# Kernel tuning notes

Hardware: AMD Instinct MI355X
Metric: run time of the kernel (lower is better)

## Reference

```python
import jax, jax.numpy as jnp
import numpy as np

K = 3          # conv kernel size
STRIDE = 1     # conv stride (SAME padding)
ITERS = 3      # DR routing iterations
EPS = 1e-9     # squash epsilon


def squash(s, axis):
    # v = ||s||^2 / (1 + ||s||^2) * s / ||s||   (DR squash)
    sq = jnp.sum(s * s, axis=axis, keepdims=True)
    return (sq / (1.0 + sq)) * s * jax.lax.rsqrt(sq + EPS)


def setup_inputs() -> dict:
    key = jax.random.key(0)
    k1, k2, k3 = jax.random.split(key, 3)
    b, h, w, iCaps, iPose = 8, 12, 12, 32, 16
    oCaps, oPose = 32, 16
    x = jax.random.normal(k1, (b, h, w, iCaps, iPose), dtype=jnp.float32)
    # Wa: [kk*iCaps, oCaps, iPose, oPose] (leading 1 of the TF weight is dropped)
    fan = K * K * iCaps * iPose
    W = jax.random.normal(k2, (K * K * iCaps, oCaps, iPose, oPose), dtype=jnp.float32) * np.float32(np.sqrt(2.0 / fan))
    # biases: [oCaps, oPose] (TF shape [1,1,oCaps,oPose,1], broadcastable)
    biases = jax.random.normal(k3, (oCaps, oPose), dtype=jnp.float32) * 0.05
    return {"x": x, "W": W, "biases": biases}


def _kernel_tile(x2d):
    # im2col for SAME padding, stride 1.  x2d: (b, h, w, C) -> (b, h, w, k*k, C)
    b, h, w, C = x2d.shape
    pad = K // 2
    xp = jnp.pad(x2d, ((0, 0), (pad, pad), (pad, pad), (0, 0)))
    patches = jnp.stack(
        [xp[:, i:i + h, j:j + w, :] for i in range(K) for j in range(K)], axis=3
    )
    return patches  # (b, h, w, k*k, C)


def reference(x, W, biases):
    b, h, w, iCaps, iPose = x.shape
    iC = K * K * iCaps
    oC, oP = biases.shape

    # 1. kernel_tile: gather k*k neighborhoods
    patches = _kernel_tile(x.reshape(b, h, w, iCaps * iPose))      # (b,h,w,kk,iCaps*iPose)
    u = patches.reshape(b * h * w, iC, iPose)                       # (bx, iC, iPose)

    # 2. transform_view (vector capsules): votes[n,i,c,:] = u[n,i,:] @ W[i,c,:,:]
    votes = jnp.einsum('nip,icpq->nicq', u, W)                      # (bx, iC, oC, oP)

    # 3. DR routing
    bx = votes.shape[0]
    logits = jnp.zeros((bx, iC, oC), dtype=votes.dtype)
    v = None
    for ii in range(ITERS):
        c = jax.nn.softmax(logits, axis=2)                          # coupling coeffs over oCaps
        s = jnp.einsum('nic,nicq->ncq', c, votes) + biases          # (bx, oC, oP)
        v = squash(s, axis=2)
        if ii < ITERS - 1:
            logits = logits + jnp.einsum('nicq,ncq->nic', votes, v)  # agreement

    return v.reshape(b, h, w, oC, oP)
```

## Files before the change

### kernel.cpp

```cpp
#include <hip/hip_runtime.h>
#include <stdint.h>

typedef unsigned short ushort_t;

#define KK3 3
#define IC 32
#define IP 16
#define OC 32
#define OP 16
#define NI 288
#define HH 12
#define WWW 12
#define NTOT 1152
#define CQ 512
#define EPSQ 1e-9f
#define RWAVES 4
#define RSTEPS 36
#define NIP 144
#define NIG 18
#define IPG 8
#define SROW 132
#define SPAR (16 * SROW)
#define SWAVE (2 * SPAR)

typedef __attribute__((ext_vector_type(8))) short bf16x8;
typedef __attribute__((ext_vector_type(4))) float f32x4;

__device__ __forceinline__ float bf_lo(unsigned u) { return __uint_as_float(u << 16); }
__device__ __forceinline__ float bf_hi(unsigned u) { return __uint_as_float(u & 0xffff0000u); }
__device__ __forceinline__ ushort_t f2bf(float f) {
    unsigned u = __float_as_uint(f);
    return (ushort_t)((u + 0x7fffu + ((u >> 16) & 1u)) >> 16);
}

__global__ __launch_bounds__(64) void pack_kernel(
    const float* __restrict__ W, ushort_t* __restrict__ Wp)
{
    const int blk = blockIdx.x;
    const int ip = blk >> 5;
    const int c = blk & 31;
    const int l = threadIdx.x;
    const int i = ip * 2 + ((l >> 5) & 1);
    const int p0 = ((l >> 4) & 1) * 8;
    const int q = l & 15;
    const float* src = W + (((size_t)(i * 32 + c) * 16 + p0) * 16 + q);
    union { ushort_t s[8]; uint4 u4; } o;
#pragma unroll
    for (int j = 0; j < 8; ++j) o.s[j] = f2bf(src[(size_t)j * 16]);
    *(uint4*)(Wp + ((size_t)blk * 64 + l) * 8) = o.u4;
}

__global__ __launch_bounds__(256) void votes_s0_kernel(
    const float* __restrict__ x, const ushort_t* __restrict__ Wp,
    ushort_t* __restrict__ votes, float* __restrict__ s0_part,
    int nStart, int nCount)
{
    __shared__ ushort_t slab[4 * SWAVE];

    const int t = threadIdx.x;
    const int w = t >> 6;
    const int l = t & 63;
    const int pxt = blockIdx.x;
    const int ig = blockIdx.y;

    const int n = nStart + pxt * 16 + (l & 15);
    const int b = n / (HH * WWW);
    const int rem = n % (HH * WWW);
    const int y = rem / WWW;
    const int xx = rem % WWW;
    const int ioff = (l >> 5) & 1;
    const int p0 = ((l >> 4) & 1) * 8;

    const int q = l & 15;
    const int r0 = (l >> 4) * 4;
    const int j16 = l & 15;
    const int g4 = l >> 4;

    ushort_t* const myslab = slab + w * SWAVE;

    const bf16x8 z8 = {0, 0, 0, 0, 0, 0, 0, 0};
    const f32x4 z4 = {0.f, 0.f, 0.f, 0.f};

    f32x4 accs0[8];
#pragma unroll
    for (int ctl = 0; ctl < 8; ++ctl) accs0[ctl] = z4;

    for (int m = 0; m < IPG; ++m) {
        const int ip = ig * IPG + m;
        union { ushort_t s[8]; bf16x8 v; } ua;
        {
            const int i = ip * 2 + ioff;
            const int ky = i / (KK3 * IC);
            const int kx = (i / IC) % KK3;
            const int ic = i & (IC - 1);
            const int sy = y + ky - 1;
            const int sx = xx + kx - 1;
            if (sy >= 0 && sy < HH && sx >= 0 && sx < WWW) {
                const float* s = x + ((((size_t)b * HH + sy) * WWW + sx) * IC + ic) * IP + p0;
                const float4 v0 = *(const float4*)s;
                const float4 v1 = *(const float4*)(s + 4);
                ua.s[0] = f2bf(v0.x); ua.s[1] = f2bf(v0.y); ua.s[2] = f2bf(v0.z); ua.s[3] = f2bf(v0.w);
                ua.s[4] = f2bf(v1.x); ua.s[5] = f2bf(v1.y); ua.s[6] = f2bf(v1.z); ua.s[7] = f2bf(v1.w);
            } else {
#pragma unroll
                for (int j = 0; j < 8; ++j) ua.s[j] = 0;
            }
        }

#pragma unroll
        for (int ctl = 0; ctl < 8; ++ctl) {
            const int ct = w * 8 + ctl;
            const bf16x8 frag = *(const bf16x8*)(Wp + (((size_t)ip * 32 + ct) * 64 + l) * 8);
            const bf16x8 be = (l < 32) ? frag : z8;
            const bf16x8 bo = (l < 32) ? z8 : frag;
            const f32x4 ve = __builtin_amdgcn_mfma_f32_16x16x32_bf16(ua.v, be, z4, 0, 0, 0);
            const f32x4 vo = __builtin_amdgcn_mfma_f32_16x16x32_bf16(ua.v, bo, z4, 0, 0, 0);
            accs0[ctl] = __builtin_amdgcn_mfma_f32_16x16x32_bf16(ua.v, frag, accs0[ctl], 0, 0, 0);
#pragma unroll
            for (int r = 0; r < 4; ++r) {
                myslab[(r0 + r) * SROW + ctl * 16 + q] = f2bf(ve[r]);
                myslab[SPAR + (r0 + r) * SROW + ctl * 16 + q] = f2bf(vo[r]);
            }
        }

#pragma unroll
        for (int s = 0; s < 2; ++s) {
#pragma unroll
            for (int h = 0; h < 4; ++h) {
                const int row = h * 4 + g4;
                const ushort_t* sp = myslab + s * SPAR + row * SROW + j16 * 8;
                const uint2 lo = *(const uint2*)sp;
                const uint2 hi = *(const uint2*)(sp + 4);
                ushort_t* dst = votes + ((size_t)(pxt * 16 + row) * NI + (2 * ip + s)) * CQ
                                + w * 128 + j16 * 8;
                uint4 o; o.x = lo.x; o.y = lo.y; o.z = hi.x; o.w = hi.y;
                *(uint4*)dst = o;
            }
        }
    }

    {
#pragma unroll
        for (int ctl = 0; ctl < 8; ++ctl) {
            const int cq = (w * 8 + ctl) * 16 + q;
#pragma unroll
            for (int r = 0; r < 4; ++r)
                s0_part[((size_t)ig * nCount + pxt * 16 + r0 + r) * CQ + cq] = accs0[ctl][r];
        }
    }
}

#define UNPACK16(A, B)                                                     \
    const float f0 = bf_lo(A.x), f1 = bf_hi(A.x), f2 = bf_lo(A.y),         \
                f3 = bf_hi(A.y), f4 = bf_lo(A.z), f5 = bf_hi(A.z),         \
                f6 = bf_lo(A.w), f7 = bf_hi(A.w), f8 = bf_lo(B.x),         \
                f9 = bf_hi(B.x), f10 = bf_lo(B.y), f11 = bf_hi(B.y),       \
                f12 = bf_lo(B.z), f13 = bf_hi(B.z), f14 = bf_lo(B.w),      \
                f15 = bf_hi(B.w);

__global__ __launch_bounds__(256) void route_kernel(
    const ushort_t* __restrict__ votes, const float* __restrict__ s0_part,
    const float* __restrict__ bias, float* __restrict__ out,
    int nStart, int nCount)
{
    __shared__ float sPart[RWAVES][CQ];
    __shared__ float s_sh[CQ];
    __shared__ float vcur_sh[CQ];
    __shared__ float fac_sh[OC];
    __shared__ float pad_lds[5632];

    const int bn = blockIdx.x;
    const int t = threadIdx.x;
    ((volatile float*)pad_lds)[t] = 0.f;

    const int wv = t >> 6;
    const int l = t & 63;
    const int isub = l >> 5;
    const int c = l & 31;
    const int iBase = 2 * wv + isub;

    const ushort_t* pbase = votes + (size_t)bn * NI * CQ + (size_t)iBase * CQ + c * OP;
    const size_t stepB = (size_t)8 * CQ;

#pragma unroll
    for (int rep = 0; rep < 2; ++rep) {
        const int k = t + rep * 256;
        float s = 0.f;
#pragma unroll
        for (int g = 0; g < NIG; ++g)
            s += s0_part[((size_t)g * nCount + bn) * CQ + k];
        s_sh[k] = fmaf(s, 1.0f / OC, bias[k]);
    }
    __syncthreads();
    if (t < OC) {
        float sq = 0.f;
#pragma unroll
        for (int q = 0; q < OP; ++q) { const float s = s_sh[t * OP + q]; sq = fmaf(s, s, sq); }
        fac_sh[t] = (sq / (1.0f + sq)) * rsqrtf(sq + EPSQ);
    }
    __syncthreads();
#pragma unroll
    for (int rep = 0; rep < 2; ++rep) {
        const int k = t + rep * 256;
        vcur_sh[k] = s_sh[k] * fac_sh[k >> 4];
    }
    __syncthreads();

    float sa[16];
    float vr[16];

#define RBODY(AA, BB)                                                       \
        {                                                                   \
            UNPACK16(AA, BB)                                                \
            float a = f0 * vr[0];                                           \
            a = fmaf(f1, vr[1], a);   a = fmaf(f2, vr[2], a);               \
            a = fmaf(f3, vr[3], a);   a = fmaf(f4, vr[4], a);               \
            a = fmaf(f5, vr[5], a);   a = fmaf(f6, vr[6], a);               \
            a = fmaf(f7, vr[7], a);   a = fmaf(f8, vr[8], a);               \
            a = fmaf(f9, vr[9], a);   a = fmaf(f10, vr[10], a);             \
            a = fmaf(f11, vr[11], a); a = fmaf(f12, vr[12], a);             \
            a = fmaf(f13, vr[13], a); a = fmaf(f14, vr[14], a);             \
            a = fmaf(f15, vr[15], a);                                       \
            const float e = __expf(a);                                      \
            float es = e;                                                   \
            es += __shfl_xor(es, 1);                                        \
            es += __shfl_xor(es, 2);                                        \
            es += __shfl_xor(es, 4);                                        \
            es += __shfl_xor(es, 8);                                        \
            es += __shfl_xor(es, 16);                                       \
            const float coup = __fdividef(e, es);                           \
            sa[0] = fmaf(coup, f0, sa[0]);   sa[1] = fmaf(coup, f1, sa[1]); \
            sa[2] = fmaf(coup, f2, sa[2]);   sa[3] = fmaf(coup, f3, sa[3]); \
            sa[4] = fmaf(coup, f4, sa[4]);   sa[5] = fmaf(coup, f5, sa[5]); \
            sa[6] = fmaf(coup, f6, sa[6]);   sa[7] = fmaf(coup, f7, sa[7]); \
            sa[8] = fmaf(coup, f8, sa[8]);   sa[9] = fmaf(coup, f9, sa[9]); \
            sa[10] = fmaf(coup, f10, sa[10]); sa[11] = fmaf(coup, f11, sa[11]); \
            sa[12] = fmaf(coup, f12, sa[12]); sa[13] = fmaf(coup, f13, sa[13]); \
            sa[14] = fmaf(coup, f14, sa[14]); sa[15] = fmaf(coup, f15, sa[15]); \
        }
#define RPREF(AA, BB, rn)                                                   \
        if ((rn) < RSTEPS) {                                                \
            const uint4* pn = (const uint4*)(pbase + (size_t)(rn) * stepB); \
            AA = pn[0]; BB = pn[1];                                         \
        }

#pragma unroll
    for (int it = 0; it < 2; ++it) {
#pragma unroll
        for (int k = 0; k < 4; ++k) {
            const float4 v4 = *(const float4*)&vcur_sh[c * 16 + 4 * k];
            vr[4*k] = v4.x; vr[4*k+1] = v4.y; vr[4*k+2] = v4.z; vr[4*k+3] = v4.w;
        }
#pragma unroll
        for (int q = 0; q < 16; ++q) sa[q] = 0.f;

        uint4 A0, B0, A1, B1, A2, B2, A3, B3, A4, B4, A5, B5;
        RPREF(A0, B0, 0)
        RPREF(A1, B1, 1)
        RPREF(A2, B2, 2)
        RPREF(A3, B3, 3)
        RPREF(A4, B4, 4)
        RPREF(A5, B5, 5)
        for (int r = 0; r < RSTEPS; r += 6) {
            RBODY(A0, B0) RPREF(A0, B0, r + 6)
            RBODY(A1, B1) RPREF(A1, B1, r + 7)
            RBODY(A2, B2) RPREF(A2, B2, r + 8)
            RBODY(A3, B3) RPREF(A3, B3, r + 9)
            RBODY(A4, B4) RPREF(A4, B4, r + 10)
            RBODY(A5, B5) RPREF(A5, B5, r + 11)
        }

#pragma unroll
        for (int q = 0; q < 16; ++q) sa[q] += __shfl_xor(sa[q], 32);
        if (isub == 0) {
#pragma unroll
            for (int k = 0; k < 4; ++k)
                *(float4*)&sPart[wv][c * 16 + 4 * k] = make_float4(sa[4*k], sa[4*k+1], sa[4*k+2], sa[4*k+3]);
        }
        __syncthreads();
#pragma unroll
        for (int rep = 0; rep < 2; ++rep) {
            const int k = t + rep * 256;
            float s = (sPart[0][k] + sPart[1][k]) + (sPart[2][k] + sPart[3][k]);
            s_sh[k] = s + bias[k];
        }
        __syncthreads();
        if (t < OC) {
            float sq = 0.f;
#pragma unroll
            for (int q = 0; q < OP; ++q) { const float s = s_sh[t * OP + q]; sq = fmaf(s, s, sq); }
            fac_sh[t] = (sq / (1.0f + sq)) * rsqrtf(sq + EPSQ);
        }
        __syncthreads();
        if (it == 0) {
#pragma unroll
            for (int rep = 0; rep < 2; ++rep) {
                const int k = t + rep * 256;
                vcur_sh[k] += s_sh[k] * fac_sh[k >> 4];
            }
            __syncthreads();
        } else {
#pragma unroll
            for (int rep = 0; rep < 2; ++rep) {
                const int k = t + rep * 256;
                out[(size_t)(nStart + bn) * CQ + k] = s_sh[k] * fac_sh[k >> 4];
            }
        }
    }
}

extern "C" void kernel_launch(void* const* d_in, const int* in_sizes, int n_in,
                              void* d_out, int out_size, void* d_ws, size_t ws_size,
                              hipStream_t stream)
{
    const float* x = (const float*)d_in[0];
    const float* Wg = (const float*)d_in[1];
    const float* bias = (const float*)d_in[2];
    float* out = (float*)d_out;

    const size_t perN = (size_t)NI * CQ * sizeof(ushort_t);
    const size_t packBytes = (size_t)NIP * 32 * 64 * 8 * 2;
    const size_t perNpart = (size_t)NIG * CQ * sizeof(float);

    int chunk = 768;
    if (ws_size < (size_t)chunk * (perN + perNpart) + packBytes) {
        size_t avail = (ws_size > packBytes) ? ws_size - packBytes : 0;
        chunk = (int)(avail / (perN + perNpart));
        chunk &= ~15;
        if (chunk < 16) chunk = 16;
    }
    const size_t packOff = (size_t)chunk * perN;
    const size_t partOff = packOff + packBytes;

    ushort_t* votes = (ushort_t*)d_ws;
    ushort_t* Wp = (ushort_t*)((char*)d_ws + packOff);
    float* s0_part = (float*)((char*)d_ws + partOff);

    hipLaunchKernelGGL(pack_kernel, dim3(NIP * 32), dim3(64), 0, stream, Wg, Wp);

    for (int start = 0; start < NTOT; start += chunk) {
        const int cnt = (NTOT - start < chunk) ? (NTOT - start) : chunk;
        hipLaunchKernelGGL(votes_s0_kernel, dim3(cnt / 16, NIG), dim3(256), 0, stream,
                           x, Wp, votes, s0_part, start, cnt);
        hipLaunchKernelGGL(route_kernel, dim3(cnt), dim3(256), 0, stream,
                           votes, s0_part, bias, out, start, cnt);
    }
}
```

Measured before the change: 246.4 us.

## Split routing into per-iteration sweep kernels over two input-capsule halves

The single route kernel, which ran both routing iterations per pixel in one block, is replaced by two sweep-kernel launches. Each launch uses a grid of pixels by two halves of the 288 input capsules, so twice as many blocks share the votes reads. Per-half partial sums go through global workspace buffers and a small final kernel applies bias and squash. This raises parallelism and occupancy at the cost of extra launches, extra global traffic for partials, and recomputing the initial s0 reduction in every block.

```diff
diff --git a/kernel.cpp b/kernel.cpp
--- a/kernel.cpp
+++ b/kernel.cpp
@@ -15,7 +15,7 @@
 #define CQ 512
 #define EPSQ 1e-9f
 #define RWAVES 4
-#define RSTEPS 36
+#define RSTEPS 18
 #define NIP 144
 #define NIG 18
 #define IPG 8
@@ -158,10 +158,10 @@
                 f12 = bf_lo(B.z), f13 = bf_hi(B.z), f14 = bf_lo(B.w),      \
                 f15 = bf_hi(B.w);
 
-__global__ __launch_bounds__(256) void route_kernel(
+__global__ __launch_bounds__(256) void sweep_kernel(
     const ushort_t* __restrict__ votes, const float* __restrict__ s0_part,
-    const float* __restrict__ bias, float* __restrict__ out,
-    int nStart, int nCount)
+    const float* __restrict__ sIn_part, float* __restrict__ sOut_part,
+    const float* __restrict__ bias, int it, int nCount)
 {
     __shared__ float sPart[RWAVES][CQ];
     __shared__ float s_sh[CQ];
@@ -170,6 +170,7 @@
     __shared__ float pad_lds[5632];
 
     const int bn = blockIdx.x;
+    const int h = blockIdx.y;
     const int t = threadIdx.x;
     ((volatile float*)pad_lds)[t] = 0.f;
 
@@ -179,7 +180,8 @@
     const int c = l & 31;
     const int iBase = 2 * wv + isub;
 
-    const ushort_t* pbase = votes + (size_t)bn * NI * CQ + (size_t)iBase * CQ + c * OP;
+    const ushort_t* pbase = votes + (size_t)bn * NI * CQ
+                            + (size_t)(h * 144 + iBase) * CQ + c * OP;
     const size_t stepB = (size_t)8 * CQ;
 
 #pragma unroll
@@ -205,9 +207,39 @@
         vcur_sh[k] = s_sh[k] * fac_sh[k >> 4];
     }
     __syncthreads();
+    if (it == 1) {
+#pragma unroll
+        for (int rep = 0; rep < 2; ++rep) {
+            const int k = t + rep * 256;
+            const float s = sIn_part[(size_t)bn * CQ + k]
+                          + sIn_part[((size_t)nCount + bn) * CQ + k] + bias[k];
+            s_sh[k] = s;
+        }
+        __syncthreads();
+        if (t < OC) {
+            float sq = 0.f;
+#pragma unroll
+            for (int q = 0; q < OP; ++q) { const float s = s_sh[t * OP + q]; sq = fmaf(s, s, sq); }
+            fac_sh[t] = (sq / (1.0f + sq)) * rsqrtf(sq + EPSQ);
+        }
+        __syncthreads();
+#pragma unroll
+        for (int rep = 0; rep < 2; ++rep) {
+            const int k = t + rep * 256;
+            vcur_sh[k] += s_sh[k] * fac_sh[k >> 4];
+        }
+        __syncthreads();
+    }
 
     float sa[16];
     float vr[16];
+#pragma unroll
+    for (int k = 0; k < 4; ++k) {
+        const float4 v4 = *(const float4*)&vcur_sh[c * 16 + 4 * k];
+        vr[4*k] = v4.x; vr[4*k+1] = v4.y; vr[4*k+2] = v4.z; vr[4*k+3] = v4.w;
+    }
+#pragma unroll
+    for (int q = 0; q < 16; ++q) sa[q] = 0.f;
 
 #define RBODY(AA, BB)                                                       \
         {                                                                   \
@@ -244,69 +276,68 @@
             AA = pn[0]; BB = pn[1];                                         \
         }
 
-#pragma unroll
-    for (int it = 0; it < 2; ++it) {
-#pragma unroll
-        for (int k = 0; k < 4; ++k) {
-            const float4 v4 = *(const float4*)&vcur_sh[c * 16 + 4 * k];
-            vr[4*k] = v4.x; vr[4*k+1] = v4.y; vr[4*k+2] = v4.z; vr[4*k+3] = v4.w;
-        }
-#pragma unroll
-        for (int q = 0; q < 16; ++q) sa[q] = 0.f;
-
-        uint4 A0, B0, A1, B1, A2, B2, A3, B3, A4, B4, A5, B5;
-        RPREF(A0, B0, 0)
-        RPREF(A1, B1, 1)
-        RPREF(A2, B2, 2)
-        RPREF(A3, B3, 3)
-        RPREF(A4, B4, 4)
-        RPREF(A5, B5, 5)
-        for (int r = 0; r < RSTEPS; r += 6) {
-            RBODY(A0, B0) RPREF(A0, B0, r + 6)
-            RBODY(A1, B1) RPREF(A1, B1, r + 7)
-            RBODY(A2, B2) RPREF(A2, B2, r + 8)
-            RBODY(A3, B3) RPREF(A3, B3, r + 9)
-            RBODY(A4, B4) RPREF(A4, B4, r + 10)
-            RBODY(A5, B5) RPREF(A5, B5, r + 11)
-        }
-
-#pragma unroll
-        for (int q = 0; q < 16; ++q) sa[q] += __shfl_xor(sa[q], 32);
-        if (isub == 0) {
-#pragma unroll
-            for (int k = 0; k < 4; ++k)
-                *(float4*)&sPart[wv][c * 16 + 4 * k] = make_float4(sa[4*k], sa[4*k+1], sa[4*k+2], sa[4*k+3]);
-        }
-        __syncthreads();
-#pragma unroll
-        for (int rep = 0; rep < 2; ++rep) {
-            const int k = t + rep * 256;
-            float s = (sPart[0][k] + sPart[1][k]) + (sPart[2][k] + sPart[3][k]);
-            s_sh[k] = s + bias[k];
-        }
-        __syncthreads();
-        if (t < OC) {
-            float sq = 0.f;
-#pragma unroll
-            for (int q = 0; q < OP; ++q) { const float s = s_sh[t * OP + q]; sq = fmaf(s, s, sq); }
-            fac_sh[t] = (sq / (1.0f + sq)) * rsqrtf(sq + EPSQ);
-        }
-        __syncthreads();
-        if (it == 0) {
-#pragma unroll
-            for (int rep = 0; rep < 2; ++rep) {
-                const int k = t + rep * 256;
-                vcur_sh[k] += s_sh[k] * fac_sh[k >> 4];
-            }
-            __syncthreads();
-        } else {
-#pragma unroll
-            for (int rep = 0; rep < 2; ++rep) {
-                const int k = t + rep * 256;
-                out[(size_t)(nStart + bn) * CQ + k] = s_sh[k] * fac_sh[k >> 4];
-            }
-        }
-    }
+    uint4 A0, B0, A1, B1, A2, B2, A3, B3, A4, B4, A5, B5;
+    RPREF(A0, B0, 0)
+    RPREF(A1, B1, 1)
+    RPREF(A2, B2, 2)
+    RPREF(A3, B3, 3)
+    RPREF(A4, B4, 4)
+    RPREF(A5, B5, 5)
+    for (int r = 0; r < RSTEPS; r += 6) {
+        RBODY(A0, B0) RPREF(A0, B0, r + 6)
+        RBODY(A1, B1) RPREF(A1, B1, r + 7)
+        RBODY(A2, B2) RPREF(A2, B2, r + 8)
+        RBODY(A3, B3) RPREF(A3, B3, r + 9)
+        RBODY(A4, B4) RPREF(A4, B4, r + 10)
+        RBODY(A5, B5) RPREF(A5, B5, r + 11)
+    }
+
+#pragma unroll
+    for (int q = 0; q < 16; ++q) sa[q] += __shfl_xor(sa[q], 32);
+    if (isub == 0) {
+#pragma unroll
+        for (int k = 0; k < 4; ++k)
+            *(float4*)&sPart[wv][c * 16 + 4 * k] = make_float4(sa[4*k], sa[4*k+1], sa[4*k+2], sa[4*k+3]);
+    }
+    __syncthreads();
+#pragma unroll
+    for (int rep = 0; rep < 2; ++rep) {
+        const int k = t + rep * 256;
+        sOut_part[((size_t)h * nCount + bn) * CQ + k] =
+            (sPart[0][k] + sPart[1][k]) + (sPart[2][k] + sPart[3][k]);
+    }
+}
+
+__global__ __launch_bounds__(64) void final_kernel(
+    const float* __restrict__ sIn_part, const float* __restrict__ bias,
+    float* __restrict__ out, int nStart, int nCount)
+{
+    const int bn = blockIdx.x;
+    const int l = threadIdx.x;
+    const int base = (l >> 1) * 16 + (l & 1) * 8;
+
+    float s[8];
+    {
+        const float4 a0 = *(const float4*)&sIn_part[(size_t)bn * CQ + base];
+        const float4 a1 = *(const float4*)&sIn_part[(size_t)bn * CQ + base + 4];
+        const float4 b0 = *(const float4*)&sIn_part[((size_t)nCount + bn) * CQ + base];
+        const float4 b1 = *(const float4*)&sIn_part[((size_t)nCount + bn) * CQ + base + 4];
+        const float4 c0 = *(const float4*)&bias[base];
+        const float4 c1 = *(const float4*)&bias[base + 4];
+        s[0] = a0.x + b0.x + c0.x; s[1] = a0.y + b0.y + c0.y;
+        s[2] = a0.z + b0.z + c0.z; s[3] = a0.w + b0.w + c0.w;
+        s[4] = a1.x + b1.x + c1.x; s[5] = a1.y + b1.y + c1.y;
+        s[6] = a1.z + b1.z + c1.z; s[7] = a1.w + b1.w + c1.w;
+    }
+    float sq = 0.f;
+#pragma unroll
+    for (int j = 0; j < 8; ++j) sq = fmaf(s[j], s[j], sq);
+    sq += __shfl_xor(sq, 1);
+    const float fac = (sq / (1.0f + sq)) * rsqrtf(sq + EPSQ);
+    float4 o0 = make_float4(s[0] * fac, s[1] * fac, s[2] * fac, s[3] * fac);
+    float4 o1 = make_float4(s[4] * fac, s[5] * fac, s[6] * fac, s[7] * fac);
+    *(float4*)&out[(size_t)(nStart + bn) * CQ + base] = o0;
+    *(float4*)&out[(size_t)(nStart + bn) * CQ + base + 4] = o1;
 }
 
 extern "C" void kernel_launch(void* const* d_in, const int* in_sizes, int n_in,
@@ -321,20 +352,25 @@
     const size_t perN = (size_t)NI * CQ * sizeof(ushort_t);
     const size_t packBytes = (size_t)NIP * 32 * 64 * 8 * 2;
     const size_t perNpart = (size_t)NIG * CQ * sizeof(float);
+    const size_t perNsw = (size_t)4 * CQ * sizeof(float);
 
     int chunk = 768;
-    if (ws_size < (size_t)chunk * (perN + perNpart) + packBytes) {
+    if (ws_size < (size_t)chunk * (perN + perNpart + perNsw) + packBytes) {
         size_t avail = (ws_size > packBytes) ? ws_size - packBytes : 0;
-        chunk = (int)(avail / (perN + perNpart));
+        chunk = (int)(avail / (perN + perNpart + perNsw));
         chunk &= ~15;
         if (chunk < 16) chunk = 16;
     }
     const size_t packOff = (size_t)chunk * perN;
     const size_t partOff = packOff + packBytes;
+    const size_t swAOff = partOff + (size_t)chunk * perNpart;
+    const size_t swBOff = swAOff + (size_t)chunk * 2 * CQ * sizeof(float);
 
     ushort_t* votes = (ushort_t*)d_ws;
     ushort_t* Wp = (ushort_t*)((char*)d_ws + packOff);
     float* s0_part = (float*)((char*)d_ws + partOff);
+    float* swA = (float*)((char*)d_ws + swAOff);
+    float* swB = (float*)((char*)d_ws + swBOff);
 
     hipLaunchKernelGGL(pack_kernel, dim3(NIP * 32), dim3(64), 0, stream, Wg, Wp);
 
@@ -342,7 +378,11 @@
         const int cnt = (NTOT - start < chunk) ? (NTOT - start) : chunk;
         hipLaunchKernelGGL(votes_s0_kernel, dim3(cnt / 16, NIG), dim3(256), 0, stream,
                            x, Wp, votes, s0_part, start, cnt);
-        hipLaunchKernelGGL(route_kernel, dim3(cnt), dim3(256), 0, stream,
-                           votes, s0_part, bias, out, start, cnt);
-    }
-}
+        hipLaunchKernelGGL(sweep_kernel, dim3(cnt, 2), dim3(256), 0, stream,
+                           votes, s0_part, swB, swA, bias, 0, cnt);
+        hipLaunchKernelGGL(sweep_kernel, dim3(cnt, 2), dim3(256), 0, stream,
+                           votes, s0_part, swA, swB, bias, 1, cnt);
+        hipLaunchKernelGGL(final_kernel, dim3(cnt), dim3(64), 0, stream,
+                           swB, bias, out, start, cnt);
+    }
+}
```

After: 280.6 us. 1.14x slower.

## Fuse votes and routing into one software-pipelined kernel with double-buffered votes

Applied to the files above, without the earlier changes.

Replaces the separate votes and routing kernels with one fused kernel whose grid mixes block roles. Each launch routes the previous chunk while computing votes for the next chunk into a second buffer, so the two phases overlap. The first-iteration s0 sum moves into dedicated blocks that run a full-K MFMA reduction in the first launch, replacing the per-group partial sums. Those blocks write s0 once per pixel, and the votes blocks drop their third MFMA. Chunk size and the IPG/NIG split change. The costs are a doubled votes workspace, an extra launch, and heterogeneous blocks that share a larger fixed LDS allocation.

```diff
diff --git a/kernel.cpp b/kernel.cpp
--- a/kernel.cpp
+++ b/kernel.cpp
@@ -17,11 +17,12 @@
 #define RWAVES 4
 #define RSTEPS 36
 #define NIP 144
-#define NIG 18
-#define IPG 8
+#define NIG 24
+#define IPG 6
 #define SROW 132
 #define SPAR (16 * SROW)
 #define SWAVE (2 * SPAR)
+#define NS0 1152
 
 typedef __attribute__((ext_vector_type(8))) short bf16x8;
 typedef __attribute__((ext_vector_type(4))) float f32x4;
@@ -50,106 +51,6 @@
     *(uint4*)(Wp + ((size_t)blk * 64 + l) * 8) = o.u4;
 }
 
-__global__ __launch_bounds__(256) void votes_s0_kernel(
-    const float* __restrict__ x, const ushort_t* __restrict__ Wp,
-    ushort_t* __restrict__ votes, float* __restrict__ s0_part,
-    int nStart, int nCount)
-{
-    __shared__ ushort_t slab[4 * SWAVE];
-
-    const int t = threadIdx.x;
-    const int w = t >> 6;
-    const int l = t & 63;
-    const int pxt = blockIdx.x;
-    const int ig = blockIdx.y;
-
-    const int n = nStart + pxt * 16 + (l & 15);
-    const int b = n / (HH * WWW);
-    const int rem = n % (HH * WWW);
-    const int y = rem / WWW;
-    const int xx = rem % WWW;
-    const int ioff = (l >> 5) & 1;
-    const int p0 = ((l >> 4) & 1) * 8;
-
-    const int q = l & 15;
-    const int r0 = (l >> 4) * 4;
-    const int j16 = l & 15;
-    const int g4 = l >> 4;
-
-    ushort_t* const myslab = slab + w * SWAVE;
-
-    const bf16x8 z8 = {0, 0, 0, 0, 0, 0, 0, 0};
-    const f32x4 z4 = {0.f, 0.f, 0.f, 0.f};
-
-    f32x4 accs0[8];
-#pragma unroll
-    for (int ctl = 0; ctl < 8; ++ctl) accs0[ctl] = z4;
-
-    for (int m = 0; m < IPG; ++m) {
-        const int ip = ig * IPG + m;
-        union { ushort_t s[8]; bf16x8 v; } ua;
-        {
-            const int i = ip * 2 + ioff;
-            const int ky = i / (KK3 * IC);
-            const int kx = (i / IC) % KK3;
-            const int ic = i & (IC - 1);
-            const int sy = y + ky - 1;
-            const int sx = xx + kx - 1;
-            if (sy >= 0 && sy < HH && sx >= 0 && sx < WWW) {
-                const float* s = x + ((((size_t)b * HH + sy) * WWW + sx) * IC + ic) * IP + p0;
-                const float4 v0 = *(const float4*)s;
-                const float4 v1 = *(const float4*)(s + 4);
-                ua.s[0] = f2bf(v0.x); ua.s[1] = f2bf(v0.y); ua.s[2] = f2bf(v0.z); ua.s[3] = f2bf(v0.w);
-                ua.s[4] = f2bf(v1.x); ua.s[5] = f2bf(v1.y); ua.s[6] = f2bf(v1.z); ua.s[7] = f2bf(v1.w);
-            } else {
-#pragma unroll
-                for (int j = 0; j < 8; ++j) ua.s[j] = 0;
-            }
-        }
-
-#pragma unroll
-        for (int ctl = 0; ctl < 8; ++ctl) {
-            const int ct = w * 8 + ctl;
-            const bf16x8 frag = *(const bf16x8*)(Wp + (((size_t)ip * 32 + ct) * 64 + l) * 8);
-            const bf16x8 be = (l < 32) ? frag : z8;
-            const bf16x8 bo = (l < 32) ? z8 : frag;
-            const f32x4 ve = __builtin_amdgcn_mfma_f32_16x16x32_bf16(ua.v, be, z4, 0, 0, 0);
-            const f32x4 vo = __builtin_amdgcn_mfma_f32_16x16x32_bf16(ua.v, bo, z4, 0, 0, 0);
-            accs0[ctl] = __builtin_amdgcn_mfma_f32_16x16x32_bf16(ua.v, frag, accs0[ctl], 0, 0, 0);
-#pragma unroll
-            for (int r = 0; r < 4; ++r) {
-                myslab[(r0 + r) * SROW + ctl * 16 + q] = f2bf(ve[r]);
-                myslab[SPAR + (r0 + r) * SROW + ctl * 16 + q] = f2bf(vo[r]);
-            }
-        }
-
-#pragma unroll
-        for (int s = 0; s < 2; ++s) {
-#pragma unroll
-            for (int h = 0; h < 4; ++h) {
-                const int row = h * 4 + g4;
-                const ushort_t* sp = myslab + s * SPAR + row * SROW + j16 * 8;
-                const uint2 lo = *(const uint2*)sp;
-                const uint2 hi = *(const uint2*)(sp + 4);
-                ushort_t* dst = votes + ((size_t)(pxt * 16 + row) * NI + (2 * ip + s)) * CQ
-                                + w * 128 + j16 * 8;
-                uint4 o; o.x = lo.x; o.y = lo.y; o.z = hi.x; o.w = hi.y;
-                *(uint4*)dst = o;
-            }
-        }
-    }
-
-    {
-#pragma unroll
-        for (int ctl = 0; ctl < 8; ++ctl) {
-            const int cq = (w * 8 + ctl) * 16 + q;
-#pragma unroll
-            for (int r = 0; r < 4; ++r)
-                s0_part[((size_t)ig * nCount + pxt * 16 + r0 + r) * CQ + cq] = accs0[ctl][r];
-        }
-    }
-}
-
 #define UNPACK16(A, B)                                                     \
     const float f0 = bf_lo(A.x), f1 = bf_hi(A.x), f2 = bf_lo(A.y),         \
                 f3 = bf_hi(A.y), f4 = bf_lo(A.z), f5 = bf_hi(A.z),         \
@@ -158,56 +59,60 @@
                 f12 = bf_lo(B.z), f13 = bf_hi(B.z), f14 = bf_lo(B.w),      \
                 f15 = bf_hi(B.w);
 
-__global__ __launch_bounds__(256) void route_kernel(
-    const ushort_t* __restrict__ votes, const float* __restrict__ s0_part,
-    const float* __restrict__ bias, float* __restrict__ out,
-    int nStart, int nCount)
+struct RouteSh {
+    float sPart[RWAVES][CQ];
+    float s_sh[CQ];
+    float vcur[CQ];
+    float fac[OC];
+};
+
+__global__ __launch_bounds__(256) void fused_kernel(
+    const float* __restrict__ x, const ushort_t* __restrict__ Wp,
+    ushort_t* __restrict__ votesW, const ushort_t* __restrict__ votesR,
+    float* __restrict__ s0_pre, const float* __restrict__ bias,
+    float* __restrict__ out,
+    int nStartV, int cntV, int nStartR, int cntR)
 {
-    __shared__ float sPart[RWAVES][CQ];
-    __shared__ float s_sh[CQ];
-    __shared__ float vcur_sh[CQ];
-    __shared__ float fac_sh[OC];
-    __shared__ float pad_lds[5632];
-
-    const int bn = blockIdx.x;
+    __shared__ __align__(16) char shmem[33792];
+
+    int bid = blockIdx.x;
     const int t = threadIdx.x;
-    ((volatile float*)pad_lds)[t] = 0.f;
-
-    const int wv = t >> 6;
+    const int w = t >> 6;
     const int l = t & 63;
-    const int isub = l >> 5;
-    const int c = l & 31;
-    const int iBase = 2 * wv + isub;
-
-    const ushort_t* pbase = votes + (size_t)bn * NI * CQ + (size_t)iBase * CQ + c * OP;
-    const size_t stepB = (size_t)8 * CQ;
-
-#pragma unroll
-    for (int rep = 0; rep < 2; ++rep) {
-        const int k = t + rep * 256;
-        float s = 0.f;
-#pragma unroll
-        for (int g = 0; g < NIG; ++g)
-            s += s0_part[((size_t)g * nCount + bn) * CQ + k];
-        s_sh[k] = fmaf(s, 1.0f / OC, bias[k]);
-    }
-    __syncthreads();
-    if (t < OC) {
-        float sq = 0.f;
-#pragma unroll
-        for (int q = 0; q < OP; ++q) { const float s = s_sh[t * OP + q]; sq = fmaf(s, s, sq); }
-        fac_sh[t] = (sq / (1.0f + sq)) * rsqrtf(sq + EPSQ);
-    }
-    __syncthreads();
-#pragma unroll
-    for (int rep = 0; rep < 2; ++rep) {
-        const int k = t + rep * 256;
-        vcur_sh[k] = s_sh[k] * fac_sh[k >> 4];
-    }
-    __syncthreads();
-
-    float sa[16];
-    float vr[16];
+
+    if (bid < cntR) {
+        RouteSh* sh = (RouteSh*)shmem;
+        const int bn = bid;
+        const int wv = w;
+        const int isub = l >> 5;
+        const int c = l & 31;
+        const int iBase = 2 * wv + isub;
+
+        const ushort_t* pbase = votesR + (size_t)bn * NI * CQ + (size_t)iBase * CQ + c * OP;
+        const size_t stepB = (size_t)8 * CQ;
+
+#pragma unroll
+        for (int rep = 0; rep < 2; ++rep) {
+            const int k = t + rep * 256;
+            sh->s_sh[k] = fmaf(s0_pre[(size_t)(nStartR + bn) * CQ + k], 1.0f / OC, bias[k]);
+        }
+        __syncthreads();
+        if (t < OC) {
+            float sq = 0.f;
+#pragma unroll
+            for (int q = 0; q < OP; ++q) { const float s = sh->s_sh[t * OP + q]; sq = fmaf(s, s, sq); }
+            sh->fac[t] = (sq / (1.0f + sq)) * rsqrtf(sq + EPSQ);
+        }
+        __syncthreads();
+#pragma unroll
+        for (int rep = 0; rep < 2; ++rep) {
+            const int k = t + rep * 256;
+            sh->vcur[k] = sh->s_sh[k] * sh->fac[k >> 4];
+        }
+        __syncthreads();
+
+        float sa[16];
+        float vr[16];
 
 #define RBODY(AA, BB)                                                       \
         {                                                                   \
@@ -245,66 +150,213 @@
         }
 
 #pragma unroll
-    for (int it = 0; it < 2; ++it) {
-#pragma unroll
-        for (int k = 0; k < 4; ++k) {
-            const float4 v4 = *(const float4*)&vcur_sh[c * 16 + 4 * k];
-            vr[4*k] = v4.x; vr[4*k+1] = v4.y; vr[4*k+2] = v4.z; vr[4*k+3] = v4.w;
-        }
-#pragma unroll
-        for (int q = 0; q < 16; ++q) sa[q] = 0.f;
-
-        uint4 A0, B0, A1, B1, A2, B2, A3, B3, A4, B4, A5, B5;
-        RPREF(A0, B0, 0)
-        RPREF(A1, B1, 1)
-        RPREF(A2, B2, 2)
-        RPREF(A3, B3, 3)
-        RPREF(A4, B4, 4)
-        RPREF(A5, B5, 5)
-        for (int r = 0; r < RSTEPS; r += 6) {
-            RBODY(A0, B0) RPREF(A0, B0, r + 6)
-            RBODY(A1, B1) RPREF(A1, B1, r + 7)
-            RBODY(A2, B2) RPREF(A2, B2, r + 8)
-            RBODY(A3, B3) RPREF(A3, B3, r + 9)
-            RBODY(A4, B4) RPREF(A4, B4, r + 10)
-            RBODY(A5, B5) RPREF(A5, B5, r + 11)
-        }
-
-#pragma unroll
-        for (int q = 0; q < 16; ++q) sa[q] += __shfl_xor(sa[q], 32);
-        if (isub == 0) {
-#pragma unroll
-            for (int k = 0; k < 4; ++k)
-                *(float4*)&sPart[wv][c * 16 + 4 * k] = make_float4(sa[4*k], sa[4*k+1], sa[4*k+2], sa[4*k+3]);
+        for (int it = 0; it < 2; ++it) {
+#pragma unroll
+            for (int k = 0; k < 4; ++k) {
+                const float4 v4 = *(const float4*)&sh->vcur[c * 16 + 4 * k];
+                vr[4*k] = v4.x; vr[4*k+1] = v4.y; vr[4*k+2] = v4.z; vr[4*k+3] = v4.w;
+            }
+#pragma unroll
+            for (int q = 0; q < 16; ++q) sa[q] = 0.f;
+
+            uint4 A0, B0, A1, B1, A2, B2, A3, B3, A4, B4, A5, B5;
+            RPREF(A0, B0, 0)
+            RPREF(A1, B1, 1)
+            RPREF(A2, B2, 2)
+            RPREF(A3, B3, 3)
+            RPREF(A4, B4, 4)
+            RPREF(A5, B5, 5)
+            for (int r = 0; r < RSTEPS; r += 6) {
+                RBODY(A0, B0) RPREF(A0, B0, r + 6)
+                RBODY(A1, B1) RPREF(A1, B1, r + 7)
+                RBODY(A2, B2) RPREF(A2, B2, r + 8)
+                RBODY(A3, B3) RPREF(A3, B3, r + 9)
+                RBODY(A4, B4) RPREF(A4, B4, r + 10)
+                RBODY(A5, B5) RPREF(A5, B5, r + 11)
+            }
+
+#pragma unroll
+            for (int q = 0; q < 16; ++q) sa[q] += __shfl_xor(sa[q], 32);
+            if (isub == 0) {
+#pragma unroll
+                for (int k = 0; k < 4; ++k)
+                    *(float4*)&sh->sPart[wv][c * 16 + 4 * k] =
+                        make_float4(sa[4*k], sa[4*k+1], sa[4*k+2], sa[4*k+3]);
+            }
+            __syncthreads();
+#pragma unroll
+            for (int rep = 0; rep < 2; ++rep) {
+                const int k = t + rep * 256;
+                float s = (sh->sPart[0][k] + sh->sPart[1][k]) + (sh->sPart[2][k] + sh->sPart[3][k]);
+                sh->s_sh[k] = s + bias[k];
+            }
+            __syncthreads();
+            if (t < OC) {
+                float sq = 0.f;
+#pragma unroll
+                for (int q = 0; q < OP; ++q) { const float s = sh->s_sh[t * OP + q]; sq = fmaf(s, s, sq); }
+                sh->fac[t] = (sq / (1.0f + sq)) * rsqrtf(sq + EPSQ);
+            }
+            __syncthreads();
+            if (it == 0) {
+#pragma unroll
+                for (int rep = 0; rep < 2; ++rep) {
+                    const int k = t + rep * 256;
+                    sh->vcur[k] += sh->s_sh[k] * sh->fac[k >> 4];
+                }
+                __syncthreads();
+            } else {
+#pragma unroll
+                for (int rep = 0; rep < 2; ++rep) {
+                    const int k = t + rep * 256;
+                    out[(size_t)(nStartR + bn) * CQ + k] = sh->s_sh[k] * sh->fac[k >> 4];
+                }
+            }
+        }
+        return;
+    }
+    bid -= cntR;
+
+    const int nvBlocks = (cntV >> 4) * NIG;
+    if (bid < nvBlocks) {
+        ushort_t* const slab = (ushort_t*)shmem;
+        const int pxt = bid / NIG;
+        const int ig = bid % NIG;
+
+        const int n = nStartV + pxt * 16 + (l & 15);
+        const int b = n / (HH * WWW);
+        const int rem = n % (HH * WWW);
+        const int y = rem / WWW;
+        const int xx = rem % WWW;
+        const int ioff = (l >> 5) & 1;
+        const int p0 = ((l >> 4) & 1) * 8;
+
+        const int q = l & 15;
+        const int r0 = (l >> 4) * 4;
+        const int j16 = l & 15;
+        const int g4 = l >> 4;
+
+        ushort_t* const myslab = slab + w * SWAVE;
+
+        const bf16x8 z8 = {0, 0, 0, 0, 0, 0, 0, 0};
+        const f32x4 z4 = {0.f, 0.f, 0.f, 0.f};
+
+        for (int m = 0; m < IPG; ++m) {
+            const int ip = ig * IPG + m;
+            union { ushort_t s[8]; bf16x8 v; } ua;
+            {
+                const int i = ip * 2 + ioff;
+                const int ky = i / (KK3 * IC);
+                const int kx = (i / IC) % KK3;
+                const int ic = i & (IC - 1);
+                const int sy = y + ky - 1;
+                const int sx = xx + kx - 1;
+                if (sy >= 0 && sy < HH && sx >= 0 && sx < WWW) {
+                    const float* s = x + ((((size_t)b * HH + sy) * WWW + sx) * IC + ic) * IP + p0;
+                    const float4 v0 = *(const float4*)s;
+                    const float4 v1 = *(const float4*)(s + 4);
+                    ua.s[0] = f2bf(v0.x); ua.s[1] = f2bf(v0.y); ua.s[2] = f2bf(v0.z); ua.s[3] = f2bf(v0.w);
+                    ua.s[4] = f2bf(v1.x); ua.s[5] = f2bf(v1.y); ua.s[6] = f2bf(v1.z); ua.s[7] = f2bf(v1.w);
+                } else {
+#pragma unroll
+                    for (int j = 0; j < 8; ++j) ua.s[j] = 0;
+                }
+            }
+
+#pragma unroll
+            for (int ctl = 0; ctl < 8; ++ctl) {
+                const int ct = w * 8 + ctl;
+                const bf16x8 frag = *(const bf16x8*)(Wp + (((size_t)ip * 32 + ct) * 64 + l) * 8);
+                const bf16x8 be = (l < 32) ? frag : z8;
+                const bf16x8 bo = (l < 32) ? z8 : frag;
+                const f32x4 ve = __builtin_amdgcn_mfma_f32_16x16x32_bf16(ua.v, be, z4, 0, 0, 0);
+                const f32x4 vo = __builtin_amdgcn_mfma_f32_16x16x32_bf16(ua.v, bo, z4, 0, 0, 0);
+#pragma unroll
+                for (int r = 0; r < 4; ++r) {
+                    myslab[(r0 + r) * SROW + ctl * 16 + q] = f2bf(ve[r]);
+                    myslab[SPAR + (r0 + r) * SROW + ctl * 16 + q] = f2bf(vo[r]);
+                }
+            }
+
+#pragma unroll
+            for (int s = 0; s < 2; ++s) {
+#pragma unroll
+                for (int h = 0; h < 4; ++h) {
+                    const int row = h * 4 + g4;
+                    const ushort_t* sp = myslab + s * SPAR + row * SROW + j16 * 8;
+                    const uint2 lo = *(const uint2*)sp;
+                    const uint2 hi = *(const uint2*)(sp + 4);
+                    ushort_t* dst = votesW + ((size_t)(pxt * 16 + row) * NI + (2 * ip + s)) * CQ
+                                    + w * 128 + j16 * 8;
+                    uint4 o; o.x = lo.x; o.y = lo.y; o.z = hi.x; o.w = hi.y;
+                    *(uint4*)dst = o;
+                }
+            }
+        }
+        return;
+    }
+    bid -= nvBlocks;
+
+    {
+        float (*red)[CQ] = (float (*)[CQ])shmem;
+
+        const int pxt = bid % (NTOT / 16);
+        const int ctb = (bid / (NTOT / 16)) * 2;
+        const int px = pxt * 16 + (l & 15);
+        const int b = px / (HH * WWW);
+        const int rem = px % (HH * WWW);
+        const int y = rem / WWW;
+        const int xx = rem % WWW;
+        const int ioff = (l >> 5) & 1;
+        const int p0 = ((l >> 4) & 1) * 8;
+
+        f32x4 acc0 = (f32x4){0.f, 0.f, 0.f, 0.f};
+        f32x4 acc1 = (f32x4){0.f, 0.f, 0.f, 0.f};
+
+        const int ip0 = w * (NIP / 4);
+        for (int k = 0; k < NIP / 4; ++k) {
+            const int ip = ip0 + k;
+            const int i = ip * 2 + ioff;
+            const int ky = i / (KK3 * IC);
+            const int kx = (i / IC) % KK3;
+            const int ic = i & (IC - 1);
+            const int sy = y + ky - 1;
+            const int sx = xx + kx - 1;
+            union { ushort_t s[8]; bf16x8 v; } ua;
+            if (sy >= 0 && sy < HH && sx >= 0 && sx < WWW) {
+                const float* s = x + ((((size_t)b * HH + sy) * WWW + sx) * IC + ic) * IP + p0;
+                const float4 v0 = *(const float4*)s;
+                const float4 v1 = *(const float4*)(s + 4);
+                ua.s[0] = f2bf(v0.x); ua.s[1] = f2bf(v0.y); ua.s[2] = f2bf(v0.z); ua.s[3] = f2bf(v0.w);
+                ua.s[4] = f2bf(v1.x); ua.s[5] = f2bf(v1.y); ua.s[6] = f2bf(v1.z); ua.s[7] = f2bf(v1.w);
+            } else {
+#pragma unroll
+                for (int j = 0; j < 8; ++j) ua.s[j] = 0;
+            }
+            const bf16x8 b0 = *(const bf16x8*)(Wp + (((size_t)ip * 32 + ctb) * 64 + l) * 8);
+            const bf16x8 b1 = *(const bf16x8*)(Wp + (((size_t)ip * 32 + ctb + 1) * 64 + l) * 8);
+            acc0 = __builtin_amdgcn_mfma_f32_16x16x32_bf16(ua.v, b0, acc0, 0, 0, 0);
+            acc1 = __builtin_amdgcn_mfma_f32_16x16x32_bf16(ua.v, b1, acc1, 0, 0, 0);
+        }
+
+        {
+            const int row = (l >> 4) * 4;
+            const int col = l & 15;
+#pragma unroll
+            for (int r = 0; r < 4; ++r) {
+                red[w][(row + r) * 16 + col] = acc0[r];
+                red[w][256 + (row + r) * 16 + col] = acc1[r];
+            }
         }
         __syncthreads();
 #pragma unroll
         for (int rep = 0; rep < 2; ++rep) {
             const int k = t + rep * 256;
-            float s = (sPart[0][k] + sPart[1][k]) + (sPart[2][k] + sPart[3][k]);
-            s_sh[k] = s + bias[k];
-        }
-        __syncthreads();
-        if (t < OC) {
-            float sq = 0.f;
-#pragma unroll
-            for (int q = 0; q < OP; ++q) { const float s = s_sh[t * OP + q]; sq = fmaf(s, s, sq); }
-            fac_sh[t] = (sq / (1.0f + sq)) * rsqrtf(sq + EPSQ);
-        }
-        __syncthreads();
-        if (it == 0) {
-#pragma unroll
-            for (int rep = 0; rep < 2; ++rep) {
-                const int k = t + rep * 256;
-                vcur_sh[k] += s_sh[k] * fac_sh[k >> 4];
-            }
-            __syncthreads();
-        } else {
-#pragma unroll
-            for (int rep = 0; rep < 2; ++rep) {
-                const int k = t + rep * 256;
-                out[(size_t)(nStart + bn) * CQ + k] = s_sh[k] * fac_sh[k >> 4];
-            }
+            const float v = (red[0][k] + red[1][k]) + (red[2][k] + red[3][k]);
+            const int ct = k >> 8;
+            const int row = (k >> 4) & 15;
+            const int col = k & 15;
+            s0_pre[(size_t)(pxt * 16 + row) * CQ + (size_t)(ctb + ct) * 16 + col] = v;
         }
     }
 }
@@ -320,29 +372,36 @@
 
     const size_t perN = (size_t)NI * CQ * sizeof(ushort_t);
     const size_t packBytes = (size_t)NIP * 32 * 64 * 8 * 2;
-    const size_t perNpart = (size_t)NIG * CQ * sizeof(float);
-
-    int chunk = 768;
-    if (ws_size < (size_t)chunk * (perN + perNpart) + packBytes) {
-        size_t avail = (ws_size > packBytes) ? ws_size - packBytes : 0;
-        chunk = (int)(avail / (perN + perNpart));
+    const size_t s0Bytes = (size_t)NTOT * CQ * sizeof(float);
+
+    int chunk = 384;
+    if (ws_size < 2 * (size_t)chunk * perN + packBytes + s0Bytes) {
+        size_t avail = (ws_size > packBytes + s0Bytes) ? ws_size - packBytes - s0Bytes : 0;
+        chunk = (int)(avail / (2 * perN));
         chunk &= ~15;
         if (chunk < 16) chunk = 16;
     }
-    const size_t packOff = (size_t)chunk * perN;
-    const size_t partOff = packOff + packBytes;
-
-    ushort_t* votes = (ushort_t*)d_ws;
-    ushort_t* Wp = (ushort_t*)((char*)d_ws + packOff);
-    float* s0_part = (float*)((char*)d_ws + partOff);
+
+    ushort_t* buf0 = (ushort_t*)d_ws;
+    ushort_t* buf1 = buf0 + (size_t)chunk * NI * CQ;
+    ushort_t* Wp = (ushort_t*)((char*)d_ws + 2 * (size_t)chunk * perN);
+    float* s0_pre = (float*)((char*)Wp + packBytes);
+    ushort_t* bufs[2] = { buf0, buf1 };
 
     hipLaunchKernelGGL(pack_kernel, dim3(NIP * 32), dim3(64), 0, stream, Wg, Wp);
 
-    for (int start = 0; start < NTOT; start += chunk) {
-        const int cnt = (NTOT - start < chunk) ? (NTOT - start) : chunk;
-        hipLaunchKernelGGL(votes_s0_kernel, dim3(cnt / 16, NIG), dim3(256), 0, stream,
-                           x, Wp, votes, s0_part, start, cnt);
-        hipLaunchKernelGGL(route_kernel, dim3(cnt), dim3(256), 0, stream,
-                           votes, s0_part, bias, out, start, cnt);
+    const int nch = (NTOT + chunk - 1) / chunk;
+    for (int j = 0; j <= nch; ++j) {
+        const int sV = j * chunk;
+        const int sR = (j - 1) * chunk;
+        const int cV = (j < nch) ? ((NTOT - sV < chunk) ? NTOT - sV : chunk) : 0;
+        const int cR = (j >= 1) ? ((NTOT - sR < chunk) ? NTOT - sR : chunk) : 0;
+        const int nv = (cV >> 4) * NIG;
+        const int ns0 = (j == 0) ? NS0 : 0;
+        const int grid = cR + nv + ns0;
+        if (grid == 0) continue;
+        hipLaunchKernelGGL(fused_kernel, dim3(grid), dim3(256), 0, stream,
+                           x, Wp, bufs[j & 1], bufs[(j + 1) & 1], s0_pre, bias, out,
+                           sV, cV, sR, cR);
     }
 }
```

Result: no change. 243.6 us (-1.2%).
